# Performance work log

Measured on AMD Instinct MI355X. Metric: run time of the kernel, lower is better.

## Reference

```python
import jax, jax.numpy as jnp
import numpy as np

STATE_DIM = 32
OBS_DIM = 16
PROCESS_VAR = 1e-4
MEAS_VAR = 1e-2
B = 2048
T = 64


def setup_inputs() -> dict:
    key = jax.random.key(0)
    k1, k2, k3 = jax.random.split(key, 3)
    state0 = jax.random.normal(k1, (B, STATE_DIM), dtype=jnp.float32)
    # Initial covariance P = I (per torch __init__), broadcast over batch
    cov0 = jnp.broadcast_to(jnp.eye(STATE_DIM, dtype=jnp.float32), (B, STATE_DIM, STATE_DIM))
    measurements = jax.random.normal(k2, (B, T, OBS_DIM), dtype=jnp.float32)
    # Parameters per torch __init__: F = eye, H = randn, Q = pv*I, R = mv*I
    F = jnp.eye(STATE_DIM, dtype=jnp.float32)
    H = jax.random.normal(k3, (OBS_DIM, STATE_DIM), dtype=jnp.float32)
    Q = PROCESS_VAR * jnp.eye(STATE_DIM, dtype=jnp.float32)
    R = MEAS_VAR * jnp.eye(OBS_DIM, dtype=jnp.float32)
    return {"state0": state0, "cov0": cov0, "measurements": measurements,
            "F": F, "H": H, "Q": Q, "R": R}


def reference(state0, cov0, measurements, F, H, Q, R):
    """Run Kalman predict+update over T timesteps; return filtered states (B,T,S)."""

    def step(carry, z):
        x, P = carry  # x: (B,S), P: (B,S,S); z: (B,O)
        # --- predict ---
        x_pred = x @ F.T                                   # F @ x per batch
        P_pred = jnp.einsum('ij,bjk,lk->bil', F, P, F) + Q  # F P F^T + Q
        # --- update ---
        y = x_pred @ H.T                                   # predicted measurement (B,O)
        innov = z - y
        S = jnp.einsum('ij,bjk,lk->bil', H, P_pred, H) + R  # (B,O,O)
        S_inv = jnp.linalg.inv(S)
        K = jnp.einsum('bij,kj,bkl->bil', P_pred, H, S_inv)  # P H^T S^{-1}, (B,S,O)
        x_new = x_pred + jnp.einsum('bij,bj->bi', K, innov)
        P_new = P_pred - jnp.einsum('bij,jk,bkl->bil', K, H, P_pred)  # (I - K H) P
        return (x_new, P_new), x_new

    # scan over time axis: measurements (B,T,O) -> (T,B,O)
    (_, _), states = jax.lax.scan(step, (state0, cov0), jnp.swapaxes(measurements, 0, 1))
    return jnp.swapaxes(states, 0, 1)  # (B,T,S)
```

## Files before the change

### kernel.cpp

```cpp
#include <hip/hip_runtime.h>
#include <math.h>


#define S_DIM 32
#define O_DIM 16
#define HS 36
#define CW 8
#define NTHR 576

__device__ __forceinline__ float rdlanef(float v, int srcLane) {
    return __uint_as_float(
        (unsigned int)__builtin_amdgcn_readlane((int)__float_as_uint(v), srcLane));
}

__global__ __launch_bounds__(NTHR) void kf_fused(
    const float* __restrict__ state0,
    const float* __restrict__ cov0,
    const float* __restrict__ meas,
    const float* __restrict__ Fm,
    const float* __restrict__ Hm,
    const float* __restrict__ Qm,
    const float* __restrict__ Rm,
    float* __restrict__ out,
    int T, int B)
{
    const int tid = threadIdx.x;

    __shared__ float P  [S_DIM*33];
    __shared__ float Fs [S_DIM*33];
    __shared__ float Qs [S_DIM*33];
    __shared__ float Tp [S_DIM*33];
    __shared__ float Hs [O_DIM*HS];
    __shared__ float HQ [O_DIM*HS];
    __shared__ float HPs[O_DIM*HS];
    __shared__ float KT [2][O_DIM*33];
    __shared__ float Sg [O_DIM*17];
    __shared__ float Rs [O_DIM*17];
    __shared__ float xs [CW][32];
    __shared__ float iv [CW][16];
    __shared__ int notId, notDiag, convFlag, convT;
    __shared__ float cupad[13000];

    if (tid == 0) {
        ((volatile float*)cupad)[0] = 0.f;
        notId = 0; notDiag = 0; convFlag = 0; convT = 0;
    }

    for (int i = tid; i < S_DIM*S_DIM; i += NTHR) {
        int r = i >> 5, c = i & 31;
        P [r*33+c] = cov0[i];
        Fs[r*33+c] = Fm[i];
        Qs[r*33+c] = Qm[i];
    }
    for (int i = tid; i < O_DIM*S_DIM; i += NTHR) {
        int r = i >> 5, c = i & 31;
        Hs[r*HS+c] = Hm[i];
    }
    for (int i = tid; i < O_DIM*O_DIM; i += NTHR) {
        int r = i >> 4, c = i & 15;
        Rs[r*17+c] = Rm[i];
    }
    __syncthreads();

    {
        bool badI = false, badD = false;
        for (int i = tid; i < S_DIM*S_DIM; i += NTHR) {
            int r = i >> 5, c = i & 31;
            if (Fs[r*33+c] != ((r == c) ? 1.0f : 0.0f)) badI = true;
        }
        for (int i = tid; i < O_DIM*O_DIM; i += NTHR) {
            int r = i >> 4, c = i & 15;
            if (r != c && Rs[r*17+c] != 0.0f) badD = true;
        }
        if (badI) notId = 1;
        if (badD) notDiag = 1;
    }
    __syncthreads();
    const bool fId   = (notId == 0);
    const bool rDiag = (notDiag == 0);

    const int wv = tid >> 6;
    const int l  = tid & 63;
    const int s  = l & 31;
    const int h  = l >> 5;
    const int o  = l & 15;
    const int q  = l >> 4;
    const int wi = (wv >= 1) ? (wv - 1) : 0;
    const bool isCons = (wv >= 1);
    long bb = (long)blockIdx.x * CW + wi;
    const long b = (bb < B) ? bb : (B - 1);

    float4 h0v, h1v;
    {
        const float4* Hv = (const float4*)(Hm + o*S_DIM + q*8);
        h0v = Hv[0]; h1v = Hv[1];
    }

    float x = 0.f;
    if (isCons) {
        x = state0[b*S_DIM + s];
        if (h == 0) xs[wi][s] = x;
    }
    __syncthreads();

    auto cons_step = [&](int tstep, int bufc) {
        float za = meas[(b*T + tstep)*O_DIM + o];
        const float4* xq = (const float4*)(&xs[wi][q*8]);
        float4 xa = xq[0], xb = xq[1];
        float p = h0v.x*xa.x + h0v.y*xa.y + h0v.z*xa.z + h0v.w*xa.w
                + h1v.x*xb.x + h1v.y*xb.y + h1v.z*xb.z + h1v.w*xb.w;
        float p2 = p + __shfl_xor(p, 16, 64);
        float y  = p2 + __shfl_xor(p2, 32, 64);
        float innov = za - y;
        __builtin_amdgcn_wave_barrier();
        if (l < 16) iv[wi][o] = innov;
        __builtin_amdgcn_wave_barrier();
        const float* ivp = &iv[wi][h*8];
        const float* ktp = &KT[bufc][(h*8)*33 + s];
        float acc = 0.f;
        #pragma unroll
        for (int m = 0; m < 8; ++m) acc = fmaf(ktp[m*33], ivp[m], acc);
        float xnew = x + (acc + __shfl_xor(acc, 32, 64));
        if (h == 0) out[(b*T + tstep)*S_DIM + s] = xnew;
        __builtin_amdgcn_wave_barrier();
        if (h == 0) xs[wi][s] = xnew;
        __builtin_amdgcn_wave_barrier();
        x = xnew;
    };

    if (fId) {
        for (int i = tid; i < S_DIM*S_DIM; i += NTHR) {
            int r = i >> 5, c = i & 31;
            P[r*33+c] += Qs[r*33+c];
        }
        __syncthreads();
        if (tid < 512) {
            int r = tid >> 5, c = tid & 31;
            float a0 = 0.f, q0 = 0.f;
            for (int k = 0; k < S_DIM; ++k) {
                a0 += Hs[r*HS+k]*P [k*33+c];
                q0 += Hs[r*HS+k]*Qs[k*33+c];
            }
            HPs[r*HS+c] = a0;
            HQ [r*HS+c] = q0;
        }
        __syncthreads();
        if (tid < 256) {
            int r = tid >> 4, c = tid & 15;
            float a = Rs[r*17+c];
            const float4* hp = (const float4*)&HPs[r*HS];
            const float4* hh = (const float4*)&Hs [c*HS];
            #pragma unroll
            for (int k = 0; k < 8; ++k) {
                float4 u = hp[k], v = hh[k];
                a += u.x*v.x + u.y*v.y + u.z*v.z + u.w*v.w;
            }
            Sg[r*17+c] = a;
        }
        __syncthreads();

        if (tid < 64) __builtin_amdgcn_s_setprio(1);

        float prevK[16];
        int t = 0;
        for (; t < T; ++t) {
            const int buf = t & 1;
            if (tid < 64) {
                const int myc = tid;
                const bool isS = (myc < O_DIM);
                const bool isK = (!isS && myc < 48);
                const int hc = (myc - O_DIM) & 31;
                float a[16];
                #pragma unroll
                for (int r = 0; r < O_DIM; ++r)
                    a[r] = isS ? Sg[r*17+myc] : HPs[r*HS+hc];

                #pragma unroll
                for (int p = 0; p < O_DIM; ++p) {
                    float sp[16];
                    #pragma unroll
                    for (int r = 0; r < O_DIM; ++r) sp[r] = rdlanef(a[r], p);
                    float pinv = __builtin_amdgcn_rcpf(sp[p]);
                    float sc = a[p] * pinv;
                    #pragma unroll
                    for (int r = 0; r < O_DIM; ++r)
                        a[r] = (r == p) ? sc : fmaf(-sp[r], sc, a[r]);
                }

                float d = 0.f;
                if (isK) {
                    #pragma unroll
                    for (int r = 0; r < O_DIM; ++r) {
                        float dd = fabsf(a[r] - prevK[r]);
                        d = fmaxf(d, dd);
                        prevK[r] = a[r];
                    }
                }
                unsigned long long anyBig = __ballot(isK && (d > 1e-5f));
                if (myc == 0 && anyBig == 0ull && t >= 1) {
                    convFlag = 1; convT = t;
                }

                if (isK) {
                    const int j = myc - O_DIM;
                    #pragma unroll
                    for (int oo = 0; oo < O_DIM; ++oo) KT[buf][oo*33+j] = a[oo];
                    if (rDiag) {
                        #pragma unroll
                        for (int r = 0; r < O_DIM; ++r)
                            HPs[r*HS+j] = fmaf(Rs[r*17+r], a[r], HQ[r*HS+j]);
                    } else {
                        #pragma unroll
                        for (int r = 0; r < O_DIM; ++r) {
                            float rg = 0.f;
                            for (int k = 0; k < O_DIM; ++k) rg += Rs[r*17+k]*a[k];
                            HPs[r*HS+j] = rg + HQ[r*HS+j];
                        }
                    }
                }
            } else if (isCons && t > 0) {
                cons_step(t - 1, buf ^ 1);
            }
            __syncthreads();

            if (convFlag) break;

            if (t + 1 < T) {
                if (tid < 256) {
                    int r = tid >> 4, c = tid & 15;
                    float a = Rs[r*17+c];
                    const float4* hp = (const float4*)&HPs[r*HS];
                    const float4* hh = (const float4*)&Hs [c*HS];
                    #pragma unroll
                    for (int k = 0; k < 8; ++k) {
                        float4 u = hp[k], v = hh[k];
                        a += u.x*v.x + u.y*v.y + u.z*v.z + u.w*v.w;
                    }
                    Sg[r*17+c] = a;
                }
                __syncthreads();
            }
        }
        if (tid < 64) __builtin_amdgcn_s_setprio(0);

        if (!isCons) return;

        if (!convFlag) {
            cons_step(T - 1, (T - 1) & 1);
            return;
        }

        const int tc  = convT;
        const int bufc = tc & 1;
        float ka[16];
        #pragma unroll
        for (int j = 0; j < 16; ++j) ka[j] = KT[bufc][j*33 + s];

        float4 kc0, kc1;
        kc0.x = h ? ka[8]  : ka[0];  kc0.y = h ? ka[9]  : ka[1];
        kc0.z = h ? ka[10] : ka[2];  kc0.w = h ? ka[11] : ka[3];
        kc1.x = h ? ka[12] : ka[4];  kc1.y = h ? ka[13] : ka[5];
        kc1.z = h ? ka[14] : ka[6];  kc1.w = h ? ka[15] : ka[7];

        float mreg[16];
        #pragma unroll
        for (int j = 0; j < 16; ++j)
            mreg[j] = (s == h*16 + j) ? 1.0f : 0.0f;
        for (int oo = 0; oo < O_DIM; ++oo) {
            const float4* Hr = (const float4*)&Hs[oo*HS + h*16];
            float4 a0 = Hr[0], a1 = Hr[1], a2 = Hr[2], a3 = Hr[3];
            float k = ka[oo];
            mreg[0]  = fmaf(-k, a0.x, mreg[0]);
            mreg[1]  = fmaf(-k, a0.y, mreg[1]);
            mreg[2]  = fmaf(-k, a0.z, mreg[2]);
            mreg[3]  = fmaf(-k, a0.w, mreg[3]);
            mreg[4]  = fmaf(-k, a1.x, mreg[4]);
            mreg[5]  = fmaf(-k, a1.y, mreg[5]);
            mreg[6]  = fmaf(-k, a1.z, mreg[6]);
            mreg[7]  = fmaf(-k, a1.w, mreg[7]);
            mreg[8]  = fmaf(-k, a2.x, mreg[8]);
            mreg[9]  = fmaf(-k, a2.y, mreg[9]);
            mreg[10] = fmaf(-k, a2.z, mreg[10]);
            mreg[11] = fmaf(-k, a2.w, mreg[11]);
            mreg[12] = fmaf(-k, a3.x, mreg[12]);
            mreg[13] = fmaf(-k, a3.y, mreg[13]);
            mreg[14] = fmaf(-k, a3.z, mreg[14]);
            mreg[15] = fmaf(-k, a3.w, mreg[15]);
        }

        int t2 = tc;
        float4 zva0, zva1, zvb0, zvb1;
        {
            const float4* Zv = (const float4*)(meas + (b*T + t2)*O_DIM + h*8);
            zva0 = Zv[0]; zva1 = Zv[1];
            const int t1 = (t2 + 1 < T) ? (t2 + 1) : t2;
            const float4* Zv1 = (const float4*)(meas + (b*T + t1)*O_DIM + h*8);
            zvb0 = Zv1[0]; zvb1 = Zv1[1];
        }

        for (; t2 < T; ++t2) {
            float4 zvc0, zvc1;
            {
                const int tn = (t2 + 2 < T) ? (t2 + 2) : (T - 1);
                const float4* Zv = (const float4*)(meas + (b*T + tn)*O_DIM + h*8);
                zvc0 = Zv[0]; zvc1 = Zv[1];
            }

            const float4* xv = (const float4*)(&xs[wi][h*16]);
            float4 xa = xv[0], xb = xv[1], xc = xv[2], xd = xv[3];
            float p = mreg[0] *xa.x + mreg[1] *xa.y + mreg[2] *xa.z + mreg[3] *xa.w
                    + mreg[4] *xb.x + mreg[5] *xb.y + mreg[6] *xb.z + mreg[7] *xb.w
                    + mreg[8] *xc.x + mreg[9] *xc.y + mreg[10]*xc.z + mreg[11]*xc.w
                    + mreg[12]*xd.x + mreg[13]*xd.y + mreg[14]*xd.z + mreg[15]*xd.w;
            p += kc0.x*zva0.x + kc0.y*zva0.y + kc0.z*zva0.z + kc0.w*zva0.w
               + kc1.x*zva1.x + kc1.y*zva1.y + kc1.z*zva1.z + kc1.w*zva1.w;
            float xnew = p + __shfl_xor(p, 32, 64);

            if (h == 0) out[(b*T + t2)*S_DIM + s] = xnew;

            __builtin_amdgcn_wave_barrier();
            if (h == 0) xs[wi][s] = xnew;
            __builtin_amdgcn_wave_barrier();

            zva0 = zvb0; zva1 = zvb1;
            zvb0 = zvc0; zvb1 = zvc1;
        }
        return;
    }

    float4 f0, f1, f2, f3;
    if (isCons) {
        const float4* Fv = (const float4*)(Fm + s*S_DIM + h*16);
        f0 = Fv[0]; f1 = Fv[1]; f2 = Fv[2]; f3 = Fv[3];
    }

    for (int t = 0; t < T; ++t) {
        for (int i = tid; i < S_DIM*S_DIM; i += NTHR) {
            int r = i >> 5, c = i & 31;
            float a = 0.f;
            for (int k = 0; k < S_DIM; ++k) a += Fs[r*33+k]*P[k*33+c];
            Tp[r*33+c] = a;
        }
        __syncthreads();
        for (int i = tid; i < S_DIM*S_DIM; i += NTHR) {
            int r = i >> 5, c = i & 31;
            float a = Qs[r*33+c];
            for (int k = 0; k < S_DIM; ++k) a += Tp[r*33+k]*Fs[c*33+k];
            P[r*33+c] = a;
        }
        __syncthreads();
        if (tid < 512) {
            int r = tid >> 5, c = tid & 31;
            float a = 0.f;
            for (int k = 0; k < S_DIM; ++k) a += Hs[r*HS+k]*P[k*33+c];
            HPs[r*HS+c] = a;
        }
        __syncthreads();
        if (tid < 256) {
            int r = tid >> 4, c = tid & 15;
            float a = Rs[r*17+c];
            const float4* hp = (const float4*)&HPs[r*HS];
            const float4* hh = (const float4*)&Hs [c*HS];
            #pragma unroll
            for (int k = 0; k < 8; ++k) {
                float4 u = hp[k], v = hh[k];
                a += u.x*v.x + u.y*v.y + u.z*v.z + u.w*v.w;
            }
            Sg[r*17+c] = a;
        }
        __syncthreads();
        if (tid < 64) {
            const int myc = tid;
            const bool isS = (myc < O_DIM);
            const bool isK = (!isS && myc < 48);
            const int hc = (myc - O_DIM) & 31;
            float a[16];
            #pragma unroll
            for (int r = 0; r < O_DIM; ++r)
                a[r] = isS ? Sg[r*17+myc] : HPs[r*HS+hc];
            #pragma unroll
            for (int p = 0; p < O_DIM; ++p) {
                float sp[16];
                #pragma unroll
                for (int r = 0; r < O_DIM; ++r) sp[r] = rdlanef(a[r], p);
                float pinv = __builtin_amdgcn_rcpf(sp[p]);
                float sc = a[p] * pinv;
                #pragma unroll
                for (int r = 0; r < O_DIM; ++r)
                    a[r] = (r == p) ? sc : fmaf(-sp[r], sc, a[r]);
            }
            if (isK) {
                const int j = myc - O_DIM;
                #pragma unroll
                for (int oo = 0; oo < O_DIM; ++oo) KT[0][oo*33+j] = a[oo];
            }
        }
        __syncthreads();

        if (isCons) {
            const float4* xv = (const float4*)(&xs[wi][h*16]);
            float4 xa = xv[0], xb = xv[1], xc = xv[2], xd = xv[3];
            float pr = f0.x*xa.x + f0.y*xa.y + f0.z*xa.z + f0.w*xa.w
                     + f1.x*xb.x + f1.y*xb.y + f1.z*xb.z + f1.w*xb.w
                     + f2.x*xc.x + f2.y*xc.y + f2.z*xc.z + f2.w*xc.w
                     + f3.x*xd.x + f3.y*xd.y + f3.z*xd.z + f3.w*xd.w;
            x = pr + __shfl_xor(pr, 32, 64);
            __builtin_amdgcn_wave_barrier();
            if (h == 0) xs[wi][s] = x;
            __builtin_amdgcn_wave_barrier();
            cons_step(t, 0);
        }

        for (int i = tid; i < S_DIM*S_DIM; i += NTHR) {
            int r = i >> 5, c = i & 31;
            float acc = 0.f;
            for (int oo = 0; oo < O_DIM; ++oo)
                acc += KT[0][oo*33+r]*HPs[oo*HS+c];
            P[r*33+c] -= acc;
        }
        __syncthreads();
    }
}

extern "C" void kernel_launch(void* const* d_in, const int* in_sizes, int n_in,
                              void* d_out, int out_size, void* d_ws, size_t ws_size,
                              hipStream_t stream) {
    const float* state0 = (const float*)d_in[0];
    const float* cov0   = (const float*)d_in[1];
    const float* meas   = (const float*)d_in[2];
    const float* Fm     = (const float*)d_in[3];
    const float* Hm     = (const float*)d_in[4];
    const float* Qm     = (const float*)d_in[5];
    const float* Rm     = (const float*)d_in[6];
    float* out = (float*)d_out;

    const int B = in_sizes[0] / S_DIM;
    const int T = in_sizes[2] / (B * O_DIM);

    const int grid = (B + CW - 1) / CW;
    kf_fused<<<dim3(grid), dim3(NTHR), 0, stream>>>(
        state0, cov0, meas, Fm, Hm, Qm, Rm, out, T, B);
}
```

Baseline: 140.5 us.

## Compute next S from S inverse algebraically, skipping per-step S GEMM and barrier

The Gauss-Jordan wavefront now also runs on the identity columns (lanes 48-63), producing S^{-1}. With diagonal R, the next innovation covariance is derived in closed form as S0 + R - R S^{-1} R, where S0 = H Q H^T + R is precomputed once. This removes the 256-thread S matrix product and one __syncthreads per timestep. It uses the otherwise idle wavefront lanes and caches diag(R) in registers, at the cost of relying on an algebraic identity that may accumulate different rounding.

```diff
diff --git a/kernel.cpp b/kernel.cpp
--- a/kernel.cpp
+++ b/kernel.cpp
@@ -36,6 +36,7 @@
     __shared__ float KT [2][O_DIM*33];
     __shared__ float Sg [O_DIM*17];
     __shared__ float Rs [O_DIM*17];
+    __shared__ float S0g[O_DIM*17];
     __shared__ float xs [CW][32];
     __shared__ float iv [CW][16];
     __shared__ int notId, notDiag, convFlag, convT;
@@ -156,10 +157,32 @@
                 a += u.x*v.x + u.y*v.y + u.z*v.z + u.w*v.w;
             }
             Sg[r*17+c] = a;
-        }
-        __syncthreads();
-
-        if (tid < 64) __builtin_amdgcn_s_setprio(1);
+        } else if (tid < 512) {
+            int i = tid - 256;
+            int r = i >> 4, c = i & 15;
+            float a = Rs[r*17+c];
+            const float4* hq = (const float4*)&HQ[r*HS];
+            const float4* hh = (const float4*)&Hs[c*HS];
+            #pragma unroll
+            for (int k = 0; k < 8; ++k) {
+                float4 u = hq[k], v = hh[k];
+                a += u.x*v.x + u.y*v.y + u.z*v.z + u.w*v.w;
+            }
+            S0g[r*17+c] = a;
+        }
+        __syncthreads();
+
+        float Rd[16], s0c[16];
+        if (tid < 64) {
+            __builtin_amdgcn_s_setprio(1);
+            #pragma unroll
+            for (int r = 0; r < O_DIM; ++r) Rd[r] = Rs[r*17+r];
+            if (tid >= 48) {
+                const int lc = tid - 48;
+                #pragma unroll
+                for (int r = 0; r < O_DIM; ++r) s0c[r] = S0g[r*17+lc];
+            }
+        }
 
         float prevK[16];
         int t = 0;
@@ -168,12 +191,19 @@
             if (tid < 64) {
                 const int myc = tid;
                 const bool isS = (myc < O_DIM);
-                const bool isK = (!isS && myc < 48);
+                const bool isK = (myc >= O_DIM && myc < 48);
+                const bool isI = (myc >= 48);
                 const int hc = (myc - O_DIM) & 31;
+                const int lc = myc & 15;
                 float a[16];
                 #pragma unroll
-                for (int r = 0; r < O_DIM; ++r)
-                    a[r] = isS ? Sg[r*17+myc] : HPs[r*HS+hc];
+                for (int r = 0; r < O_DIM; ++r) {
+                    float v;
+                    if (isS)      v = Sg[r*17+myc];
+                    else if (isK) v = HPs[r*HS+hc];
+                    else          v = (r == lc) ? 1.0f : 0.0f;
+                    a[r] = v;
+                }
 
                 #pragma unroll
                 for (int p = 0; p < O_DIM; ++p) {
@@ -208,7 +238,7 @@
                     if (rDiag) {
                         #pragma unroll
                         for (int r = 0; r < O_DIM; ++r)
-                            HPs[r*HS+j] = fmaf(Rs[r*17+r], a[r], HQ[r*HS+j]);
+                            HPs[r*HS+j] = fmaf(Rd[r], a[r], HQ[r*HS+j]);
                     } else {
                         #pragma unroll
                         for (int r = 0; r < O_DIM; ++r) {
@@ -218,6 +248,15 @@
                         }
                     }
                 }
+                if (isI && rDiag) {
+                    float rc = Rd[lc];
+                    #pragma unroll
+                    for (int r = 0; r < O_DIM; ++r) {
+                        float v = fmaf(-(Rd[r]*rc), a[r], s0c[r]);
+                        if (r == lc) v += Rd[r];
+                        Sg[r*17+lc] = v;
+                    }
+                }
             } else if (isCons && t > 0) {
                 cons_step(t - 1, buf ^ 1);
             }
@@ -225,7 +264,7 @@
 
             if (convFlag) break;
 
-            if (t + 1 < T) {
+            if (!rDiag && t + 1 < T) {
                 if (tid < 256) {
                     int r = tid >> 4, c = tid & 15;
                     float a = Rs[r*17+c];
```

Measured after the change: 146.8 us. 4.5% more time.
